# Kernel tuning notes

Measured on AMD Instinct MI355X. Metric: run time of the kernel, lower is better.

## Reference

```python
import jax, jax.numpy as jnp
import numpy as np

B, S, D = 4, 2048, 1024

def setup_inputs() -> dict:
    key = jax.random.key(0)
    k1, k2, k3, k4 = jax.random.split(key, 4)
    output = jax.random.normal(k1, (B, S, D), dtype=jnp.float32)
    # nn.Linear(dim, dim, bias=False): y = x @ W.T ; store W as [D, D]
    scale = 1.0 / np.sqrt(D)
    w_q = jax.random.uniform(k2, (D, D), dtype=jnp.float32, minval=-scale, maxval=scale)
    w_k = jax.random.uniform(k3, (D, D), dtype=jnp.float32, minval=-scale, maxval=scale)
    w_v = jax.random.uniform(k4, (D, D), dtype=jnp.float32, minval=-scale, maxval=scale)
    return {"output": output, "w_q": w_q, "w_k": w_k, "w_v": w_v}

def reference(output, w_q, w_k, w_v):
    # projections: x @ W.T (torch Linear convention)
    q = jnp.einsum('bsd,ed->bse', output, w_q)
    k = jnp.einsum('bsd,ed->bse', output, w_k)
    v = jnp.einsum('bsd,ed->bse', output, w_v)
    scores = jnp.einsum('bqd,bkd->bqk', q, k)      # unscaled, no mask
    attn = jax.nn.softmax(scores, axis=-1)
    return jnp.einsum('bqk,bkd->bqd', attn, v)
```

## Files before the change

kernel.cpp:

```cpp
#include <hip/hip_runtime.h>
#include <hip/hip_bf16.h>
#include <stdint.h>


typedef __attribute__((ext_vector_type(8))) _Float16 f16x8;
typedef __attribute__((ext_vector_type(4))) float f32x4;
typedef __attribute__((ext_vector_type(4))) unsigned short u16x4;

__device__ inline unsigned short f2h(float f) {
    union { _Float16 h; unsigned short u; } x;
    x.h = (_Float16)f;
    return x.u;
}
__device__ inline float h2f(unsigned short u) {
    union { unsigned short u; _Float16 h; } x;
    x.u = u;
    return (float)x.h;
}

__device__ inline void async16(const unsigned short* g, unsigned short* l) {
    __builtin_amdgcn_global_load_lds(
        (__attribute__((address_space(1))) void*)g,
        (__attribute__((address_space(3))) void*)l, 16, 0, 0);
}

template <int MODE, int BN>
__global__ __launch_bounds__(512)
void gemm512(const unsigned short* __restrict__ A,
             const unsigned short* __restrict__ B,
             void* __restrict__ C, void* __restrict__ C2,
             int K, int ldA, int ldB, int ldC,
             long sAz, long sBz, long sCz)
{
    constexpr int NT = BN / 32;
    constexpr int BI = BN / 64;
    __shared__ __align__(16) unsigned short smem[256 * 64 + BN * 64];
    unsigned short* As = smem;
    unsigned short* Bs = smem + 256 * 64;

    const int tid  = threadIdx.x;
    const int lane = tid & 63;
    const int wave = tid >> 6;
    const int wr   = wave >> 1, wc = wave & 1;
    const int quad = lane >> 4, lrow = lane & 15;
    const int bm   = blockIdx.x, bn = blockIdx.y, z = blockIdx.z;

    const unsigned short* Az = A + (long)z * sAz;
    const unsigned short* Bz = B + (long)z * sBz;

    const unsigned short* gA[4];
    const unsigned short* gB[BI];
#pragma unroll
    for (int i = 0; i < 4; ++i) {
        const int l = tid + 512 * i;
        const int r = l >> 3;
        const int c = (l & 7) ^ (r & 7);
        gA[i] = Az + (long)(bm * 256 + r) * ldA + c * 8;
    }
#pragma unroll
    for (int i = 0; i < BI; ++i) {
        const int l = tid + 512 * i;
        const int r = l >> 3;
        const int c = (l & 7) ^ (r & 7);
        gB[i] = Bz + (long)(bn * BN + r) * ldB + c * 8;
    }

    f32x4 acc[4][NT];
#pragma unroll
    for (int i = 0; i < 4; ++i)
#pragma unroll
        for (int j = 0; j < NT; ++j)
            acc[i][j] = f32x4{0.f, 0.f, 0.f, 0.f};

    const int fr = lrow & 7;

    for (int k0 = 0; k0 < K; k0 += 64) {
#pragma unroll
        for (int i = 0; i < 4; ++i) async16(gA[i], &As[(tid + 512 * i) * 8]);
#pragma unroll
        for (int i = 0; i < BI; ++i) async16(gB[i], &Bs[(tid + 512 * i) * 8]);
#pragma unroll
        for (int i = 0; i < 4; ++i) gA[i] += 64;
#pragma unroll
        for (int i = 0; i < BI; ++i) gB[i] += 64;
        __syncthreads();

#pragma unroll
        for (int ks = 0; ks < 2; ++ks) {
            const int pc = (((ks << 2) + quad) ^ fr) * 8;
            f16x8 af[4], bf[NT];
#pragma unroll
            for (int mt = 0; mt < 4; ++mt)
                af[mt] = *(const f16x8*)&As[(wr * 64 + mt * 16 + lrow) * 64 + pc];
#pragma unroll
            for (int nt = 0; nt < NT; ++nt)
                bf[nt] = *(const f16x8*)&Bs[(wc * (BN / 2) + nt * 16 + lrow) * 64 + pc];
#pragma unroll
            for (int mt = 0; mt < 4; ++mt)
#pragma unroll
                for (int nt = 0; nt < NT; ++nt)
                    acc[mt][nt] = __builtin_amdgcn_mfma_f32_16x16x32_f16(
                        af[mt], bf[nt], acc[mt][nt], 0, 0, 0);
        }
        __syncthreads();
    }

    const int col_base = bn * BN + wc * (BN / 2);

    if (MODE != 0 || z < 2) {
        const int row_base = bm * 256 + wr * 64;
        const long zC = (long)z * sCz;
#pragma unroll
        for (int mt = 0; mt < 4; ++mt)
#pragma unroll
            for (int nt = 0; nt < NT; ++nt)
#pragma unroll
                for (int r = 0; r < 4; ++r) {
                    const int row = row_base + mt * 16 + quad * 4 + r;
                    const int col = col_base + nt * 16 + lrow;
                    if (MODE == 2)
                        ((float*)C)[zC + (long)row * ldC + col] = acc[mt][nt][r];
                    else
                        ((unsigned short*)C)[zC + (long)row * ldC + col] =
                            f2h(acc[mt][nt][r]);
                }
    } else {
        unsigned short* T = smem;
#pragma unroll
        for (int p = 0; p < 4; ++p) {
            __syncthreads();
            if (wr == p) {
#pragma unroll
                for (int mt = 0; mt < 4; ++mt)
#pragma unroll
                    for (int nt = 0; nt < NT; ++nt) {
                        const int row_l = mt * 16 + quad * 4;
                        const int col_l = wc * 64 + nt * 16 + lrow;
                        u16x4 pk = {f2h(acc[mt][nt][0]), f2h(acc[mt][nt][1]),
                                    f2h(acc[mt][nt][2]), f2h(acc[mt][nt][3])};
                        *(u16x4*)&T[col_l * 72 + row_l] = pk;
                    }
            }
            __syncthreads();
            const int c  = tid >> 2;
            const int j0 = (tid & 3) * 16;
            const int tok0 = bm * 256 + p * 64;
            const int bb = tok0 >> 11;
            const int s0 = (tok0 & 2047) + j0;
            unsigned short* dst = (unsigned short*)C2 + (long)bb * 2097152 +
                                  (long)(bn * 128 + c) * 2048 + s0;
            const unsigned short* srcT = &T[c * 72 + j0];
            *(f16x8*)dst = *(const f16x8*)srcT;
            *(f16x8*)(dst + 8) = *(const f16x8*)(srcT + 8);
        }
    }
}

__global__ __launch_bounds__(512)
void gemm_out(const unsigned short* __restrict__ A,
              const unsigned short* __restrict__ B,
              float* __restrict__ C,
              int K, int ldA, int ldB, int ldC,
              long sAz, long sBz, long sCz)
{
    constexpr int TILE_H = 256 * 64 + 64 * 64;
    __shared__ __align__(16) unsigned short smem[2 * TILE_H];

    const int tid  = threadIdx.x;
    const int lane = tid & 63;
    const int wave = tid >> 6;
    const int wr   = wave >> 1, wc = wave & 1;
    const int quad = lane >> 4, lrow = lane & 15;
    const int bm   = blockIdx.x, bn = blockIdx.y, z = blockIdx.z;

    const unsigned short* Az = A + (long)z * sAz;
    const unsigned short* Bz = B + (long)z * sBz;

    const unsigned short* gA[4];
    const unsigned short* gB1;
#pragma unroll
    for (int i = 0; i < 4; ++i) {
        const int l = tid + 512 * i;
        const int r = l >> 3;
        const int c = (l & 7) ^ (r & 7);
        gA[i] = Az + (long)(bm * 256 + r) * ldA + c * 8;
    }
    {
        const int r = tid >> 3;
        const int c = (tid & 7) ^ (r & 7);
        gB1 = Bz + (long)(bn * 64 + r) * ldB + c * 8;
    }

    f32x4 acc[4][2];
#pragma unroll
    for (int i = 0; i < 4; ++i)
#pragma unroll
        for (int j = 0; j < 2; ++j)
            acc[i][j] = f32x4{0.f, 0.f, 0.f, 0.f};

    const int fr = lrow & 7;
    const int ntiles = K >> 6;

#pragma unroll
    for (int i = 0; i < 4; ++i) async16(gA[i], &smem[(tid + 512 * i) * 8]);
    async16(gB1, &smem[256 * 64 + tid * 8]);
#pragma unroll
    for (int i = 0; i < 4; ++i) gA[i] += 64;
    gB1 += 64;
    __syncthreads();

    for (int t = 0; t < ntiles; ++t) {
        const unsigned short* As = smem + (t & 1) * TILE_H;
        const unsigned short* Bs = As + 256 * 64;

        if (t + 1 < ntiles) {
            unsigned short* nA = smem + ((t + 1) & 1) * TILE_H;
#pragma unroll
            for (int i = 0; i < 4; ++i) {
                async16(gA[i], &nA[(tid + 512 * i) * 8]);
                gA[i] += 64;
            }
            async16(gB1, &nA[256 * 64 + tid * 8]);
            gB1 += 64;
        }

#pragma unroll
        for (int ks = 0; ks < 2; ++ks) {
            const int pc = (((ks << 2) + quad) ^ fr) * 8;
            f16x8 af[4], bf[2];
#pragma unroll
            for (int mt = 0; mt < 4; ++mt)
                af[mt] = *(const f16x8*)&As[(wr * 64 + mt * 16 + lrow) * 64 + pc];
#pragma unroll
            for (int nt = 0; nt < 2; ++nt)
                bf[nt] = *(const f16x8*)&Bs[(wc * 32 + nt * 16 + lrow) * 64 + pc];
#pragma unroll
            for (int mt = 0; mt < 4; ++mt)
#pragma unroll
                for (int nt = 0; nt < 2; ++nt)
                    acc[mt][nt] = __builtin_amdgcn_mfma_f32_16x16x32_f16(
                        af[mt], bf[nt], acc[mt][nt], 0, 0, 0);
        }

        if (t + 1 < ntiles)
            __syncthreads();
    }

    const int col_base = bn * 64 + wc * 32;
    const int row_base = bm * 256 + wr * 64;
    const long zC = (long)z * sCz;
#pragma unroll
    for (int mt = 0; mt < 4; ++mt)
#pragma unroll
        for (int nt = 0; nt < 2; ++nt)
#pragma unroll
            for (int r = 0; r < 4; ++r) {
                const int row = row_base + mt * 16 + quad * 4 + r;
                const int col = col_base + nt * 16 + lrow;
                C[zC + (long)row * ldC + col] = acc[mt][nt][r];
            }
}

__global__ __launch_bounds__(256)
void cvt_all(const float* __restrict__ x, const float* __restrict__ w0,
             const float* __restrict__ w1, const float* __restrict__ w2,
             unsigned short* __restrict__ xh, unsigned short* __restrict__ wh)
{
    const int bid = blockIdx.x;
    const float* s;
    unsigned short* d;
    long i;
    if (bid < 4096) {
        s = x; d = xh;
        i = ((long)bid * 256 + threadIdx.x) * 8;
    } else {
        const int wid = bid - 4096;
        const int w = wid >> 9;
        s = (w == 0) ? w0 : (w == 1) ? w1 : w2;
        d = wh + (long)w * 1048576;
        i = ((long)(wid & 511) * 256 + threadIdx.x) * 8;
    }
    f32x4 a = *(const f32x4*)(s + i);
    f32x4 b = *(const f32x4*)(s + i + 4);
    union { unsigned short u[8]; f16x8 v; } t;
#pragma unroll
    for (int j = 0; j < 4; ++j) { t.u[j] = f2h(a[j]); t.u[4 + j] = f2h(b[j]); }
    *(f16x8*)(d + i) = t.v;
}

__global__ __launch_bounds__(256)
void softmax16(unsigned short* __restrict__ sc)
{
    const long row = blockIdx.x;
    unsigned short* srow = sc + row * 2048;
    const int tid = threadIdx.x;

    union { u16x4 p[2]; unsigned short u[8]; } in;
    in.p[0] = *(const u16x4*)(srow + tid * 8);
    in.p[1] = *(const u16x4*)(srow + tid * 8 + 4);
    float v[8];
#pragma unroll
    for (int i = 0; i < 8; ++i) v[i] = h2f(in.u[i]);

    float m = v[0];
#pragma unroll
    for (int i = 1; i < 8; ++i) m = fmaxf(m, v[i]);
#pragma unroll
    for (int off = 32; off; off >>= 1) m = fmaxf(m, __shfl_xor(m, off));

    __shared__ float redm[4], reds[4];
    if ((tid & 63) == 0) redm[tid >> 6] = m;
    __syncthreads();
    m = fmaxf(fmaxf(redm[0], redm[1]), fmaxf(redm[2], redm[3]));

    float s = 0.f;
#pragma unroll
    for (int i = 0; i < 8; ++i) { v[i] = __expf(v[i] - m); s += v[i]; }
#pragma unroll
    for (int off = 32; off; off >>= 1) s += __shfl_xor(s, off);
    if ((tid & 63) == 0) reds[tid >> 6] = s;
    __syncthreads();
    s = reds[0] + reds[1] + reds[2] + reds[3];

    const float inv = 1.f / s;
    union { unsigned short u[8]; f16x8 w; } t;
#pragma unroll
    for (int i = 0; i < 8; ++i) t.u[i] = f2h(v[i] * inv);
    *(f16x8*)(srow + tid * 8) = t.w;
}

extern "C" void kernel_launch(void* const* d_in, const int* in_sizes, int n_in,
                              void* d_out, int out_size, void* d_ws, size_t ws_size,
                              hipStream_t stream)
{
    const float* x  = (const float*)d_in[0];
    const float* wq = (const float*)d_in[1];
    const float* wk = (const float*)d_in[2];
    const float* wv = (const float*)d_in[3];
    float* out = (float*)d_out;

    char* base = (char*)d_ws;
    const bool batched = (ws_size >= 88080384UL);

    unsigned short* xh = (unsigned short*)base;
    unsigned short* wh = (unsigned short*)(base + 16777216);
    unsigned short* sc = (unsigned short*)base;
    unsigned short* q  = (unsigned short*)(base + (batched ? 33554432 : 23068672));
    unsigned short* k  = q + 8388608;
    unsigned short* vt = k + 8388608;

    cvt_all<<<5632, 256, 0, stream>>>(x, wq, wk, wv, xh, wh);

    gemm512<0, 128><<<dim3(32, 8, 3), 512, 0, stream>>>(
        xh, wh, q, vt, 1024, 1024, 1024, 1024, 0L, 1048576L, 8388608L);

    if (batched) {
        gemm512<1, 128><<<dim3(8, 16, 4), 512, 0, stream>>>(
            q, k, sc, nullptr, 1024, 1024, 1024, 2048,
            2097152L, 2097152L, 4194304L);
        softmax16<<<8192, 256, 0, stream>>>(sc);
        gemm_out<<<dim3(8, 16, 4), 512, 0, stream>>>(
            sc, vt, out, 2048, 2048, 2048, 1024,
            4194304L, 2097152L, 2097152L);
    } else {
        for (int b = 0; b < 4; ++b) {
            gemm512<1, 128><<<dim3(8, 16, 1), 512, 0, stream>>>(
                q + (long)b * 2097152, k + (long)b * 2097152, sc, nullptr,
                1024, 1024, 1024, 2048, 0L, 0L, 0L);
            softmax16<<<2048, 256, 0, stream>>>(sc);
            gemm_out<<<dim3(8, 16, 1), 512, 0, stream>>>(
                sc, vt + (long)b * 2097152, out + (long)b * 2097152,
                2048, 2048, 2048, 1024, 0L, 0L, 0L);
        }
    }
}
```

Measured before the change: 226.4 us.

## Fuse Q/K/V projections into one kernel sharing the activation tile

Adds a dedicated proj3 kernel that computes all three projections per 128x128 output tile, loading each X tile once and reusing it against the Q, K and V weight tiles. It uses double-buffered async global-to-LDS loads with a 32-wide K step, 256 threads and two blocks per CU. The V result is still written transposed through LDS. This cuts redundant X reads across the three projections and drops the MODE-0 transpose path from gemm512, at the cost of 192 accumulator registers per thread, which may limit occupancy or cause spills.

```diff
diff --git a/kernel.cpp b/kernel.cpp
--- a/kernel.cpp
+++ b/kernel.cpp
@@ -22,6 +22,147 @@
     __builtin_amdgcn_global_load_lds(
         (__attribute__((address_space(1))) void*)g,
         (__attribute__((address_space(3))) void*)l, 16, 0, 0);
+}
+
+__global__ __launch_bounds__(256, 2)
+void proj3(const unsigned short* __restrict__ xh,
+           const unsigned short* __restrict__ wh,
+           unsigned short* __restrict__ q,
+           unsigned short* __restrict__ kk,
+           unsigned short* __restrict__ vt)
+{
+    __shared__ __align__(16) unsigned short smem[2 * 16384];
+
+    const int tid  = threadIdx.x;
+    const int lane = tid & 63;
+    const int wave = tid >> 6;
+    const int wr   = wave >> 1, wc = wave & 1;
+    const int quad = lane >> 4, lrow = lane & 15;
+    const int bm   = blockIdx.x, bn = blockIdx.y;
+
+    const unsigned short* gA[2];
+    const unsigned short* gB[2];
+#pragma unroll
+    for (int i = 0; i < 2; ++i) {
+        const int l = tid + 256 * i;
+        const int r = l >> 2;
+        const int c = (l & 3) ^ ((r >> 1) & 3);
+        gA[i] = xh + (long)(bm * 128 + r) * 1024 + c * 8;
+        gB[i] = wh + (long)(bn * 128 + r) * 1024 + c * 8;
+    }
+
+    f32x4 acc[3][4][4];
+#pragma unroll
+    for (int z = 0; z < 3; ++z)
+#pragma unroll
+        for (int m = 0; m < 4; ++m)
+#pragma unroll
+            for (int n = 0; n < 4; ++n)
+                acc[z][m][n] = f32x4{0.f, 0.f, 0.f, 0.f};
+
+    const int pc = (quad ^ ((lrow >> 1) & 3)) * 8;
+
+#pragma unroll
+    for (int i = 0; i < 2; ++i)
+        async16(gA[i], &smem[(tid + 256 * i) * 8]);
+#pragma unroll
+    for (int z = 0; z < 3; ++z)
+#pragma unroll
+        for (int i = 0; i < 2; ++i)
+            async16(gB[i] + (long)z * 1048576,
+                    &smem[4096 * (1 + z) + (tid + 256 * i) * 8]);
+#pragma unroll
+    for (int i = 0; i < 2; ++i) { gA[i] += 32; gB[i] += 32; }
+    __syncthreads();
+
+    for (int t = 0; t < 32; ++t) {
+        const unsigned short* cb = smem + (t & 1) * 16384;
+
+        if (t + 1 < 32) {
+            unsigned short* nb = smem + ((t + 1) & 1) * 16384;
+#pragma unroll
+            for (int i = 0; i < 2; ++i) {
+                async16(gA[i], &nb[(tid + 256 * i) * 8]);
+                gA[i] += 32;
+            }
+#pragma unroll
+            for (int z = 0; z < 3; ++z)
+#pragma unroll
+                for (int i = 0; i < 2; ++i)
+                    async16(gB[i] + (long)z * 1048576,
+                            &nb[4096 * (1 + z) + (tid + 256 * i) * 8]);
+#pragma unroll
+            for (int i = 0; i < 2; ++i) gB[i] += 32;
+        }
+
+        f16x8 af[4];
+#pragma unroll
+        for (int mt = 0; mt < 4; ++mt)
+            af[mt] = *(const f16x8*)&cb[(wr * 64 + mt * 16 + lrow) * 32 + pc];
+#pragma unroll
+        for (int z = 0; z < 3; ++z) {
+            f16x8 bf[4];
+#pragma unroll
+            for (int nt = 0; nt < 4; ++nt)
+                bf[nt] = *(const f16x8*)
+                    &cb[4096 * (1 + z) + (wc * 64 + nt * 16 + lrow) * 32 + pc];
+#pragma unroll
+            for (int mt = 0; mt < 4; ++mt)
+#pragma unroll
+                for (int nt = 0; nt < 4; ++nt)
+                    acc[z][mt][nt] = __builtin_amdgcn_mfma_f32_16x16x32_f16(
+                        af[mt], bf[nt], acc[z][mt][nt], 0, 0, 0);
+        }
+
+        if (t + 1 < 32)
+            __syncthreads();
+    }
+
+#pragma unroll
+    for (int z = 0; z < 2; ++z) {
+        unsigned short* dst = z ? kk : q;
+#pragma unroll
+        for (int mt = 0; mt < 4; ++mt)
+#pragma unroll
+            for (int nt = 0; nt < 4; ++nt)
+#pragma unroll
+                for (int r = 0; r < 4; ++r) {
+                    const int row = bm * 128 + wr * 64 + mt * 16 + quad * 4 + r;
+                    const int col = bn * 128 + wc * 64 + nt * 16 + lrow;
+                    dst[(long)row * 1024 + col] = f2h(acc[z][mt][nt][r]);
+                }
+    }
+
+    unsigned short* T = smem;
+#pragma unroll
+    for (int p = 0; p < 2; ++p) {
+        __syncthreads();
+        if (wr == p) {
+#pragma unroll
+            for (int mt = 0; mt < 4; ++mt)
+#pragma unroll
+                for (int nt = 0; nt < 4; ++nt) {
+                    const int row_l = mt * 16 + quad * 4;
+                    const int col_l = wc * 64 + nt * 16 + lrow;
+                    u16x4 pk = {f2h(acc[2][mt][nt][0]), f2h(acc[2][mt][nt][1]),
+                                f2h(acc[2][mt][nt][2]), f2h(acc[2][mt][nt][3])};
+                    *(u16x4*)&T[col_l * 72 + row_l] = pk;
+                }
+        }
+        __syncthreads();
+        const int c  = tid >> 1;
+        const int j0 = (tid & 1) * 32;
+        const int tok0 = bm * 128 + p * 64;
+        const int bb = tok0 >> 11;
+        const int s0 = (tok0 & 2047) + j0;
+        unsigned short* dst = vt + (long)bb * 2097152 +
+                              (long)(bn * 128 + c) * 2048 + s0;
+        const unsigned short* srcT = &T[c * 72 + j0];
+        *(f16x8*)dst        = *(const f16x8*)srcT;
+        *(f16x8*)(dst + 8)  = *(const f16x8*)(srcT + 8);
+        *(f16x8*)(dst + 16) = *(const f16x8*)(srcT + 16);
+        *(f16x8*)(dst + 24) = *(const f16x8*)(srcT + 24);
+    }
 }
 
 template <int MODE, int BN>
@@ -106,54 +247,22 @@
     }
 
     const int col_base = bn * BN + wc * (BN / 2);
-
-    if (MODE != 0 || z < 2) {
-        const int row_base = bm * 256 + wr * 64;
-        const long zC = (long)z * sCz;
-#pragma unroll
-        for (int mt = 0; mt < 4; ++mt)
-#pragma unroll
-            for (int nt = 0; nt < NT; ++nt)
-#pragma unroll
-                for (int r = 0; r < 4; ++r) {
-                    const int row = row_base + mt * 16 + quad * 4 + r;
-                    const int col = col_base + nt * 16 + lrow;
-                    if (MODE == 2)
-                        ((float*)C)[zC + (long)row * ldC + col] = acc[mt][nt][r];
-                    else
-                        ((unsigned short*)C)[zC + (long)row * ldC + col] =
-                            f2h(acc[mt][nt][r]);
-                }
-    } else {
-        unsigned short* T = smem;
-#pragma unroll
-        for (int p = 0; p < 4; ++p) {
-            __syncthreads();
-            if (wr == p) {
-#pragma unroll
-                for (int mt = 0; mt < 4; ++mt)
-#pragma unroll
-                    for (int nt = 0; nt < NT; ++nt) {
-                        const int row_l = mt * 16 + quad * 4;
-                        const int col_l = wc * 64 + nt * 16 + lrow;
-                        u16x4 pk = {f2h(acc[mt][nt][0]), f2h(acc[mt][nt][1]),
-                                    f2h(acc[mt][nt][2]), f2h(acc[mt][nt][3])};
-                        *(u16x4*)&T[col_l * 72 + row_l] = pk;
-                    }
+    const int row_base = bm * 256 + wr * 64;
+    const long zC = (long)z * sCz;
+#pragma unroll
+    for (int mt = 0; mt < 4; ++mt)
+#pragma unroll
+        for (int nt = 0; nt < NT; ++nt)
+#pragma unroll
+            for (int r = 0; r < 4; ++r) {
+                const int row = row_base + mt * 16 + quad * 4 + r;
+                const int col = col_base + nt * 16 + lrow;
+                if (MODE == 2)
+                    ((float*)C)[zC + (long)row * ldC + col] = acc[mt][nt][r];
+                else
+                    ((unsigned short*)C)[zC + (long)row * ldC + col] =
+                        f2h(acc[mt][nt][r]);
             }
-            __syncthreads();
-            const int c  = tid >> 2;
-            const int j0 = (tid & 3) * 16;
-            const int tok0 = bm * 256 + p * 64;
-            const int bb = tok0 >> 11;
-            const int s0 = (tok0 & 2047) + j0;
-            unsigned short* dst = (unsigned short*)C2 + (long)bb * 2097152 +
-                                  (long)(bn * 128 + c) * 2048 + s0;
-            const unsigned short* srcT = &T[c * 72 + j0];
-            *(f16x8*)dst = *(const f16x8*)srcT;
-            *(f16x8*)(dst + 8) = *(const f16x8*)(srcT + 8);
-        }
-    }
 }
 
 __global__ __launch_bounds__(512)
@@ -351,8 +460,7 @@
 
     cvt_all<<<5632, 256, 0, stream>>>(x, wq, wk, wv, xh, wh);
 
-    gemm512<0, 128><<<dim3(32, 8, 3), 512, 0, stream>>>(
-        xh, wh, q, vt, 1024, 1024, 1024, 1024, 0L, 1048576L, 8388608L);
+    proj3<<<dim3(64, 8), 256, 0, stream>>>(xh, wh, q, k, vt);
 
     if (batched) {
         gemm512<1, 128><<<dim3(8, 16, 4), 512, 0, stream>>>(
```

Measured after the change: 237.0 us. +4.7%, slower.

## Fuse Q/K/V projections into one kernel sharing the X tile across three weights

Applied to the files above, without the earlier changes.

Replaces the z-batched projection GEMM (one 256x128 tile per weight) with a 768-thread kernel where each block loads a 128-row X tile once and computes 128x128 outputs for all three weights, with one group of four waves per projection. X is read from global memory once per block instead of three times, and loads are double-buffered in 128KB of LDS. The V output is still transposed through LDS. The smaller M tile, the larger block and the heavy LDS use may reduce occupancy. The transpose epilogue is removed from the generic gemm512.

```diff
diff --git a/kernel.cpp b/kernel.cpp
--- a/kernel.cpp
+++ b/kernel.cpp
@@ -22,6 +22,158 @@
     __builtin_amdgcn_global_load_lds(
         (__attribute__((address_space(1))) void*)g,
         (__attribute__((address_space(3))) void*)l, 16, 0, 0);
+}
+
+__global__ __launch_bounds__(768, 3)
+void proj3(const unsigned short* __restrict__ xh,
+           const unsigned short* __restrict__ wh,
+           unsigned short* __restrict__ q,
+           unsigned short* __restrict__ kk,
+           unsigned short* __restrict__ vt)
+{
+    __shared__ __align__(16) unsigned short smem[2 * 32768];
+
+    const int tid  = threadIdx.x;
+    const int lane = tid & 63;
+    const int wave = tid >> 6;
+    const int z    = wave >> 2;
+    const int wr   = (wave >> 1) & 1;
+    const int wc   = wave & 1;
+    const int quad = lane >> 4, lrow = lane & 15;
+    const int bm   = blockIdx.x, bn = blockIdx.y;
+
+    const unsigned short* gA0 = nullptr;
+    const unsigned short* gA1 = nullptr;
+    if (tid < 512) {
+#pragma unroll
+        for (int i = 0; i < 2; ++i) {
+            const int l = tid + 512 * i;
+            const int r = l >> 3;
+            const int c = (l & 7) ^ (r & 7);
+            const unsigned short* p =
+                xh + (long)(bm * 128 + r) * 1024 + c * 8;
+            if (i == 0) gA0 = p; else gA1 = p;
+        }
+    }
+    const unsigned short* gB[4];
+    int dB[4];
+#pragma unroll
+    for (int i = 0; i < 4; ++i) {
+        const int b  = tid + 768 * i;
+        const int bz = b >> 10;
+        const int l  = b & 1023;
+        const int r  = l >> 3;
+        const int c  = (l & 7) ^ (r & 7);
+        gB[i] = wh + (long)bz * 1048576 + (long)(bn * 128 + r) * 1024 + c * 8;
+        dB[i] = 8192 * (1 + bz) + l * 8;
+    }
+
+    f32x4 acc[4][4];
+#pragma unroll
+    for (int m = 0; m < 4; ++m)
+#pragma unroll
+        for (int n = 0; n < 4; ++n)
+            acc[m][n] = f32x4{0.f, 0.f, 0.f, 0.f};
+
+    const int fr = lrow & 7;
+    const int zofs = 8192 * (1 + z);
+
+    if (tid < 512) {
+        async16(gA0, &smem[tid * 8]);
+        async16(gA1, &smem[(tid + 512) * 8]);
+        gA0 += 64; gA1 += 64;
+    }
+#pragma unroll
+    for (int i = 0; i < 4; ++i) {
+        async16(gB[i], &smem[dB[i]]);
+        gB[i] += 64;
+    }
+    __syncthreads();
+
+    for (int t = 0; t < 16; ++t) {
+        const unsigned short* cb = smem + (t & 1) * 32768;
+
+        if (t + 1 < 16) {
+            unsigned short* nb = smem + ((t + 1) & 1) * 32768;
+            if (tid < 512) {
+                async16(gA0, &nb[tid * 8]);
+                async16(gA1, &nb[(tid + 512) * 8]);
+                gA0 += 64; gA1 += 64;
+            }
+#pragma unroll
+            for (int i = 0; i < 4; ++i) {
+                async16(gB[i], &nb[dB[i]]);
+                gB[i] += 64;
+            }
+        }
+
+#pragma unroll
+        for (int ks = 0; ks < 2; ++ks) {
+            const int pc = (((ks << 2) + quad) ^ fr) * 8;
+            f16x8 af[4], bf[4];
+#pragma unroll
+            for (int mt = 0; mt < 4; ++mt)
+                af[mt] = *(const f16x8*)&cb[(wr * 64 + mt * 16 + lrow) * 64 + pc];
+#pragma unroll
+            for (int nt = 0; nt < 4; ++nt)
+                bf[nt] = *(const f16x8*)
+                    &cb[zofs + (wc * 64 + nt * 16 + lrow) * 64 + pc];
+#pragma unroll
+            for (int mt = 0; mt < 4; ++mt)
+#pragma unroll
+                for (int nt = 0; nt < 4; ++nt)
+                    acc[mt][nt] = __builtin_amdgcn_mfma_f32_16x16x32_f16(
+                        af[mt], bf[nt], acc[mt][nt], 0, 0, 0);
+        }
+
+        if (t + 1 < 16)
+            __syncthreads();
+    }
+
+    if (z < 2) {
+        unsigned short* dst = z ? kk : q;
+#pragma unroll
+        for (int mt = 0; mt < 4; ++mt)
+#pragma unroll
+            for (int nt = 0; nt < 4; ++nt)
+#pragma unroll
+                for (int r = 0; r < 4; ++r) {
+                    const int row = bm * 128 + wr * 64 + mt * 16 + quad * 4 + r;
+                    const int col = bn * 128 + wc * 64 + nt * 16 + lrow;
+                    dst[(long)row * 1024 + col] = f2h(acc[mt][nt][r]);
+                }
+    }
+
+    unsigned short* T = smem;
+#pragma unroll
+    for (int p = 0; p < 2; ++p) {
+        __syncthreads();
+        if (z == 2 && wr == p) {
+#pragma unroll
+            for (int mt = 0; mt < 4; ++mt)
+#pragma unroll
+                for (int nt = 0; nt < 4; ++nt) {
+                    const int row_l = mt * 16 + quad * 4;
+                    const int col_l = wc * 64 + nt * 16 + lrow;
+                    u16x4 pk = {f2h(acc[mt][nt][0]), f2h(acc[mt][nt][1]),
+                                f2h(acc[mt][nt][2]), f2h(acc[mt][nt][3])};
+                    *(u16x4*)&T[col_l * 72 + row_l] = pk;
+                }
+        }
+        __syncthreads();
+        if (tid < 512) {
+            const int c  = tid >> 2;
+            const int j0 = (tid & 3) * 16;
+            const int tok0 = bm * 128 + p * 64;
+            const int bb = tok0 >> 11;
+            const int s0 = (tok0 & 2047) + j0;
+            unsigned short* dst = vt + (long)bb * 2097152 +
+                                  (long)(bn * 128 + c) * 2048 + s0;
+            const unsigned short* srcT = &T[c * 72 + j0];
+            *(f16x8*)dst       = *(const f16x8*)srcT;
+            *(f16x8*)(dst + 8) = *(const f16x8*)(srcT + 8);
+        }
+    }
 }
 
 template <int MODE, int BN>
@@ -106,54 +258,22 @@
     }
 
     const int col_base = bn * BN + wc * (BN / 2);
-
-    if (MODE != 0 || z < 2) {
-        const int row_base = bm * 256 + wr * 64;
-        const long zC = (long)z * sCz;
-#pragma unroll
-        for (int mt = 0; mt < 4; ++mt)
-#pragma unroll
-            for (int nt = 0; nt < NT; ++nt)
-#pragma unroll
-                for (int r = 0; r < 4; ++r) {
-                    const int row = row_base + mt * 16 + quad * 4 + r;
-                    const int col = col_base + nt * 16 + lrow;
-                    if (MODE == 2)
-                        ((float*)C)[zC + (long)row * ldC + col] = acc[mt][nt][r];
-                    else
-                        ((unsigned short*)C)[zC + (long)row * ldC + col] =
-                            f2h(acc[mt][nt][r]);
-                }
-    } else {
-        unsigned short* T = smem;
-#pragma unroll
-        for (int p = 0; p < 4; ++p) {
-            __syncthreads();
-            if (wr == p) {
-#pragma unroll
-                for (int mt = 0; mt < 4; ++mt)
-#pragma unroll
-                    for (int nt = 0; nt < NT; ++nt) {
-                        const int row_l = mt * 16 + quad * 4;
-                        const int col_l = wc * 64 + nt * 16 + lrow;
-                        u16x4 pk = {f2h(acc[mt][nt][0]), f2h(acc[mt][nt][1]),
-                                    f2h(acc[mt][nt][2]), f2h(acc[mt][nt][3])};
-                        *(u16x4*)&T[col_l * 72 + row_l] = pk;
-                    }
+    const int row_base = bm * 256 + wr * 64;
+    const long zC = (long)z * sCz;
+#pragma unroll
+    for (int mt = 0; mt < 4; ++mt)
+#pragma unroll
+        for (int nt = 0; nt < NT; ++nt)
+#pragma unroll
+            for (int r = 0; r < 4; ++r) {
+                const int row = row_base + mt * 16 + quad * 4 + r;
+                const int col = col_base + nt * 16 + lrow;
+                if (MODE == 2)
+                    ((float*)C)[zC + (long)row * ldC + col] = acc[mt][nt][r];
+                else
+                    ((unsigned short*)C)[zC + (long)row * ldC + col] =
+                        f2h(acc[mt][nt][r]);
             }
-            __syncthreads();
-            const int c  = tid >> 2;
-            const int j0 = (tid & 3) * 16;
-            const int tok0 = bm * 256 + p * 64;
-            const int bb = tok0 >> 11;
-            const int s0 = (tok0 & 2047) + j0;
-            unsigned short* dst = (unsigned short*)C2 + (long)bb * 2097152 +
-                                  (long)(bn * 128 + c) * 2048 + s0;
-            const unsigned short* srcT = &T[c * 72 + j0];
-            *(f16x8*)dst = *(const f16x8*)srcT;
-            *(f16x8*)(dst + 8) = *(const f16x8*)(srcT + 8);
-        }
-    }
 }
 
 __global__ __launch_bounds__(512)
@@ -351,8 +471,7 @@
 
     cvt_all<<<5632, 256, 0, stream>>>(x, wq, wk, wv, xh, wh);
 
-    gemm512<0, 128><<<dim3(32, 8, 3), 512, 0, stream>>>(
-        xh, wh, q, vt, 1024, 1024, 1024, 1024, 0L, 1048576L, 8388608L);
+    proj3<<<dim3(64, 8), 768, 0, stream>>>(xh, wh, q, k, vt);
 
     if (batched) {
         gemm512<1, 128><<<dim3(8, 16, 4), 512, 0, stream>>>(
```

Result: no change. 227.9 us (+0.7%).

## Double-buffer LDS tiles with K=32 steps in projection and score GEMMs

Applied to the files above, without the earlier changes.

Replaces the single-buffered K=64 tile loop with a double-buffered K=32 loop, so the async global-to-LDS load of the next tile is issued before the MFMAs on the current tile. This aims to hide global load latency and halves the barriers per iteration. The tile width and XOR swizzle are adapted to 32-column rows. The trade-off is less MFMA work per barrier and possible LDS bank-conflict changes. The unused float-output mode and the BN template parameter are removed.

```diff
diff --git a/kernel.cpp b/kernel.cpp
--- a/kernel.cpp
+++ b/kernel.cpp
@@ -24,19 +24,16 @@
         (__attribute__((address_space(3))) void*)l, 16, 0, 0);
 }
 
-template <int MODE, int BN>
+template <int MODE>
 __global__ __launch_bounds__(512)
-void gemm512(const unsigned short* __restrict__ A,
-             const unsigned short* __restrict__ B,
-             void* __restrict__ C, void* __restrict__ C2,
-             int K, int ldA, int ldB, int ldC,
-             long sAz, long sBz, long sCz)
-{
-    constexpr int NT = BN / 32;
-    constexpr int BI = BN / 64;
-    __shared__ __align__(16) unsigned short smem[256 * 64 + BN * 64];
-    unsigned short* As = smem;
-    unsigned short* Bs = smem + 256 * 64;
+void gemm512p(const unsigned short* __restrict__ A,
+              const unsigned short* __restrict__ B,
+              void* __restrict__ C, void* __restrict__ C2,
+              int K, int ldA, int ldB, int ldC,
+              long sAz, long sBz, long sCz)
+{
+    constexpr int TILE_H = 256 * 32 + 128 * 32;
+    __shared__ __align__(16) unsigned short smem[2 * TILE_H];
 
     const int tid  = threadIdx.x;
     const int lane = tid & 63;
@@ -48,64 +45,68 @@
     const unsigned short* Az = A + (long)z * sAz;
     const unsigned short* Bz = B + (long)z * sBz;
 
-    const unsigned short* gA[4];
-    const unsigned short* gB[BI];
-#pragma unroll
-    for (int i = 0; i < 4; ++i) {
+    const unsigned short* gA[2];
+    const unsigned short* gB1;
+#pragma unroll
+    for (int i = 0; i < 2; ++i) {
         const int l = tid + 512 * i;
-        const int r = l >> 3;
-        const int c = (l & 7) ^ (r & 7);
+        const int r = l >> 2;
+        const int c = (l & 3) ^ ((r >> 1) & 3);
         gA[i] = Az + (long)(bm * 256 + r) * ldA + c * 8;
     }
-#pragma unroll
-    for (int i = 0; i < BI; ++i) {
-        const int l = tid + 512 * i;
-        const int r = l >> 3;
-        const int c = (l & 7) ^ (r & 7);
-        gB[i] = Bz + (long)(bn * BN + r) * ldB + c * 8;
-    }
-
-    f32x4 acc[4][NT];
+    {
+        const int l = tid;
+        const int r = l >> 2;
+        const int c = (l & 3) ^ ((r >> 1) & 3);
+        gB1 = Bz + (long)(bn * 128 + r) * ldB + c * 8;
+    }
+
+    f32x4 acc[4][4];
 #pragma unroll
     for (int i = 0; i < 4; ++i)
 #pragma unroll
-        for (int j = 0; j < NT; ++j)
+        for (int j = 0; j < 4; ++j)
             acc[i][j] = f32x4{0.f, 0.f, 0.f, 0.f};
 
-    const int fr = lrow & 7;
-
-    for (int k0 = 0; k0 < K; k0 += 64) {
-#pragma unroll
-        for (int i = 0; i < 4; ++i) async16(gA[i], &As[(tid + 512 * i) * 8]);
-#pragma unroll
-        for (int i = 0; i < BI; ++i) async16(gB[i], &Bs[(tid + 512 * i) * 8]);
-#pragma unroll
-        for (int i = 0; i < 4; ++i) gA[i] += 64;
-#pragma unroll
-        for (int i = 0; i < BI; ++i) gB[i] += 64;
-        __syncthreads();
-
-#pragma unroll
-        for (int ks = 0; ks < 2; ++ks) {
-            const int pc = (((ks << 2) + quad) ^ fr) * 8;
-            f16x8 af[4], bf[NT];
-#pragma unroll
-            for (int mt = 0; mt < 4; ++mt)
-                af[mt] = *(const f16x8*)&As[(wr * 64 + mt * 16 + lrow) * 64 + pc];
-#pragma unroll
-            for (int nt = 0; nt < NT; ++nt)
-                bf[nt] = *(const f16x8*)&Bs[(wc * (BN / 2) + nt * 16 + lrow) * 64 + pc];
-#pragma unroll
-            for (int mt = 0; mt < 4; ++mt)
-#pragma unroll
-                for (int nt = 0; nt < NT; ++nt)
-                    acc[mt][nt] = __builtin_amdgcn_mfma_f32_16x16x32_f16(
-                        af[mt], bf[nt], acc[mt][nt], 0, 0, 0);
-        }
-        __syncthreads();
-    }
-
-    const int col_base = bn * BN + wc * (BN / 2);
+    const int pc = (quad ^ ((lrow >> 1) & 3)) * 8;
+    const int ntiles = K >> 5;
+
+    async16(gA[0], &smem[tid * 8]);
+    async16(gA[1], &smem[(tid + 512) * 8]);
+    async16(gB1, &smem[8192 + tid * 8]);
+    gA[0] += 32; gA[1] += 32; gB1 += 32;
+    __syncthreads();
+
+    for (int t = 0; t < ntiles; ++t) {
+        const unsigned short* cb = smem + (t & 1) * TILE_H;
+
+        if (t + 1 < ntiles) {
+            unsigned short* nb = smem + ((t + 1) & 1) * TILE_H;
+            async16(gA[0], &nb[tid * 8]);
+            async16(gA[1], &nb[(tid + 512) * 8]);
+            async16(gB1, &nb[8192 + tid * 8]);
+            gA[0] += 32; gA[1] += 32; gB1 += 32;
+        }
+
+        f16x8 af[4], bf[4];
+#pragma unroll
+        for (int mt = 0; mt < 4; ++mt)
+            af[mt] = *(const f16x8*)&cb[(wr * 64 + mt * 16 + lrow) * 32 + pc];
+#pragma unroll
+        for (int nt = 0; nt < 4; ++nt)
+            bf[nt] = *(const f16x8*)&cb[8192 + (wc * 64 + nt * 16 + lrow) * 32 + pc];
+#pragma unroll
+        for (int mt = 0; mt < 4; ++mt)
+#pragma unroll
+            for (int nt = 0; nt < 4; ++nt)
+                acc[mt][nt] = __builtin_amdgcn_mfma_f32_16x16x32_f16(
+                    af[mt], bf[nt], acc[mt][nt], 0, 0, 0);
+
+        if (t + 1 < ntiles)
+            __syncthreads();
+    }
+
+    const int col_base = bn * 128 + wc * 64;
 
     if (MODE != 0 || z < 2) {
         const int row_base = bm * 256 + wr * 64;
@@ -113,16 +114,13 @@
 #pragma unroll
         for (int mt = 0; mt < 4; ++mt)
 #pragma unroll
-            for (int nt = 0; nt < NT; ++nt)
+            for (int nt = 0; nt < 4; ++nt)
 #pragma unroll
                 for (int r = 0; r < 4; ++r) {
                     const int row = row_base + mt * 16 + quad * 4 + r;
                     const int col = col_base + nt * 16 + lrow;
-                    if (MODE == 2)
-                        ((float*)C)[zC + (long)row * ldC + col] = acc[mt][nt][r];
-                    else
-                        ((unsigned short*)C)[zC + (long)row * ldC + col] =
-                            f2h(acc[mt][nt][r]);
+                    ((unsigned short*)C)[zC + (long)row * ldC + col] =
+                        f2h(acc[mt][nt][r]);
                 }
     } else {
         unsigned short* T = smem;
@@ -133,7 +131,7 @@
 #pragma unroll
                 for (int mt = 0; mt < 4; ++mt)
 #pragma unroll
-                    for (int nt = 0; nt < NT; ++nt) {
+                    for (int nt = 0; nt < 4; ++nt) {
                         const int row_l = mt * 16 + quad * 4;
                         const int col_l = wc * 64 + nt * 16 + lrow;
                         u16x4 pk = {f2h(acc[mt][nt][0]), f2h(acc[mt][nt][1]),
@@ -351,11 +349,11 @@
 
     cvt_all<<<5632, 256, 0, stream>>>(x, wq, wk, wv, xh, wh);
 
-    gemm512<0, 128><<<dim3(32, 8, 3), 512, 0, stream>>>(
+    gemm512p<0><<<dim3(32, 8, 3), 512, 0, stream>>>(
         xh, wh, q, vt, 1024, 1024, 1024, 1024, 0L, 1048576L, 8388608L);
 
     if (batched) {
-        gemm512<1, 128><<<dim3(8, 16, 4), 512, 0, stream>>>(
+        gemm512p<1><<<dim3(8, 16, 4), 512, 0, stream>>>(
             q, k, sc, nullptr, 1024, 1024, 1024, 2048,
             2097152L, 2097152L, 4194304L);
         softmax16<<<8192, 256, 0, stream>>>(sc);
@@ -364,7 +362,7 @@
             4194304L, 2097152L, 2097152L);
     } else {
         for (int b = 0; b < 4; ++b) {
-            gemm512<1, 128><<<dim3(8, 16, 1), 512, 0, stream>>>(
+            gemm512p<1><<<dim3(8, 16, 1), 512, 0, stream>>>(
                 q + (long)b * 2097152, k + (long)b * 2097152, sc, nullptr,
                 1024, 1024, 1024, 2048, 0L, 0L, 0L);
             softmax16<<<2048, 256, 0, stream>>>(sc);
```

After: 242.3 us. 1.07x slower.
